# Kernel optimization log

Hardware: AMD Instinct MI355X
Metric: run time of the kernel (lower is better)

Reference implementation:

```python
import jax, jax.numpy as jnp
import numpy as np

D_MODEL = 1024
N_LAYERS = 4
EXPAND = 2
D_CONV = 4
D_STATE = 16
INTER = EXPAND * D_MODEL          # 2048
DT_RANK = (D_MODEL + 15) // 16    # 64, HF: math.ceil(d_model/16)
B_SZ = 4
SEQ = 1024
EPS = 1e-5


def setup_inputs() -> dict:
    key = jax.random.key(0)
    ks = jax.random.split(key, 8)
    nrm = lambda k, s: (0.02 * jax.random.normal(k, s)).astype(jnp.float32)
    return {
        "x": jax.random.normal(ks[0], (B_SZ, SEQ, D_MODEL), dtype=jnp.float32),
        "in_w": nrm(ks[1], (N_LAYERS, 2 * INTER, D_MODEL)),           # in_proj (no bias)
        "conv_w": nrm(ks[2], (N_LAYERS, INTER, D_CONV)),              # depthwise conv weight
        "conv_b": jnp.zeros((N_LAYERS, INTER), jnp.float32),           # conv bias
        "x_w": nrm(ks[3], (N_LAYERS, DT_RANK + 2 * D_STATE, INTER)),  # x_proj (no bias)
        "dt_w": nrm(ks[4], (N_LAYERS, INTER, DT_RANK)),               # dt_proj weight
        "dt_b": jax.random.uniform(ks[5], (N_LAYERS, INTER), minval=-4.0, maxval=-2.0).astype(jnp.float32),
        "A_log": jnp.tile(jnp.log(jnp.arange(1, D_STATE + 1, dtype=jnp.float32)), (N_LAYERS, INTER, 1)),
        "D": jnp.ones((N_LAYERS, INTER), jnp.float32),
        "out_w": nrm(ks[6], (N_LAYERS, D_MODEL, INTER)),              # out_proj (no bias)
        "norm_w": jnp.ones((N_LAYERS, D_MODEL), jnp.float32),          # per-block RMSNorm
        "norm_f_w": jnp.ones((D_MODEL,), jnp.float32),                 # final RMSNorm
    }


def _rmsnorm(x, w):
    return x * jax.lax.rsqrt(jnp.mean(x * x, axis=-1, keepdims=True) + EPS) * w


def _mixer(x, in_w, conv_w, conv_b, x_w, dt_w, dt_b, A_log, Dp, out_w):
    # x: [B, L, d_model]
    Bb = x.shape[0]
    proj = x @ in_w.T                              # [B, L, 2I]
    hs, gate = jnp.split(proj, 2, axis=-1)          # each [B, L, I]
    # causal depthwise conv over time
    hc = hs.transpose(0, 2, 1)                      # [B, I, L]
    hc = jnp.pad(hc, ((0, 0), (0, 0), (D_CONV - 1, 0)))
    hc = jax.lax.conv_general_dilated(
        hc, conv_w[:, None, :], (1,), 'VALID',
        dimension_numbers=('NCH', 'OIH', 'NCH'), feature_group_count=INTER)
    hc = hc + conv_b[None, :, None]
    u = jax.nn.silu(hc).transpose(0, 2, 1)          # [B, L, I]
    ssm = u @ x_w.T                                 # [B, L, dt_rank + 2N]
    dt, Bm, Cm = jnp.split(ssm, [DT_RANK, DT_RANK + D_STATE], axis=-1)
    dt = jax.nn.softplus(dt @ dt_w.T + dt_b)        # [B, L, I]
    A = -jnp.exp(A_log)                             # [I, N]

    def step(state, xs):
        dt_t, B_t, C_t, u_t = xs                    # [B,I], [B,N], [B,N], [B,I]
        dA = jnp.exp(dt_t[:, :, None] * A[None])    # [B, I, N]
        state = dA * state + (dt_t * u_t)[:, :, None] * B_t[:, None, :]
        y = jnp.einsum('bin,bn->bi', state, C_t)
        return state, y

    init = jnp.zeros((Bb, INTER, D_STATE), x.dtype)
    xs = (dt.transpose(1, 0, 2), Bm.transpose(1, 0, 2),
          Cm.transpose(1, 0, 2), u.transpose(1, 0, 2))
    _, ys = jax.lax.scan(step, init, xs)            # ys: [L, B, I]
    y = ys.transpose(1, 0, 2) + u * Dp              # skip term D * u
    y = y * jax.nn.silu(gate)
    return y @ out_w.T                              # [B, L, d_model]


def reference(x, in_w, conv_w, conv_b, x_w, dt_w, dt_b, A_log, D, out_w, norm_w, norm_f_w):
    h = x
    for l in range(N_LAYERS):
        h = h + _mixer(_rmsnorm(h, norm_w[l]), in_w[l], conv_w[l], conv_b[l],
                       x_w[l], dt_w[l], dt_b[l], A_log[l], D[l], out_w[l])
    return _rmsnorm(h, norm_f_w)
```

## Files before the change

### kernel.cpp

```cpp
#include <hip/hip_runtime.h>
#include <hip/hip_bf16.h>
#include <math.h>

#define D_MODEL 1024
#define N_LAYERS 4
#define INTER 2048
#define D_CONV 4
#define D_STATE 16
#define DT_RANK 64
#define B_SZ 4
#define SEQ 1024
#define TOK (B_SZ*SEQ)
#define XROWS 128
#define EPSV 1e-5f
#define GCH 64
#define TC (SEQ/GCH)
#define KSPL 4
#define OSPL 2

typedef unsigned short u16;
typedef unsigned int u32;
typedef __attribute__((ext_vector_type(8))) short bf16x8;
typedef __attribute__((ext_vector_type(4))) short s16x4;
typedef __attribute__((ext_vector_type(4))) float f32x4;

__device__ __forceinline__ u16 f2b(float f) {
    union { float f; unsigned u; } v; v.f = f;
    unsigned r = v.u + 0x7fffu + ((v.u >> 16) & 1u);
    return (u16)(r >> 16);
}
__device__ __forceinline__ float b2f(u16 h) {
    union { unsigned u; float f; } v; v.u = ((unsigned)h) << 16;
    return v.f;
}
__device__ __forceinline__ float silu(float x) {
    return x / (1.f + __expf(-x));
}
__device__ __forceinline__ void gload16(const void* g, void* l) {
    __builtin_amdgcn_global_load_lds(
        (const __attribute__((address_space(1))) void*)g,
        (__attribute__((address_space(3))) void*)l, 16, 0, 0);
}

__global__ __launch_bounds__(512, 2)
void gemm256_k(const u16* __restrict__ A, const u16* __restrict__ B,
               u16* __restrict__ C, int K, int ldc)
{
    __shared__ u16 lds[2][2][256 * 64];
    const int tid  = threadIdx.x;
    const int lane = tid & 63;
    const int wid  = tid >> 6;
    const int wr   = wid >> 2;
    const int wc   = wid & 3;
    const int row0 = blockIdx.y * 256;
    const int col0 = blockIdx.x * 256;
    const int r16   = lane & 15;
    const int khalf = lane >> 4;

    auto stage = [&](int buf, int k0) {
#pragma unroll
        for (int l = 0; l < 8; ++l) {
            int op = l >> 2;
            int c  = tid + (l & 3) * 512;
            int r  = c >> 3;
            int ds = c & 7;
            int sc = (ds ^ (r & 7)) * 8;
            const u16* src = op ? &B[(size_t)(col0 + r) * K + k0 + sc]
                                : &A[(size_t)(row0 + r) * K + k0 + sc];
            gload16(src, &lds[buf][op][c * 8]);
        }
    };
    auto rdA = [&](int buf, int mrow, int ks) -> bf16x8 {
        int row  = wr * 128 + mrow + r16;
        int phys = ((ks << 2) | khalf) ^ (row & 7);
        return *(const bf16x8*)&lds[buf][0][row * 64 + phys * 8];
    };
    auto rdB = [&](int buf, int nrow, int ks) -> bf16x8 {
        int row  = wc * 64 + nrow + r16;
        int phys = ((ks << 2) | khalf) ^ (row & 7);
        return *(const bf16x8*)&lds[buf][1][row * 64 + phys * 8];
    };

    f32x4 acc[8][4];
#pragma unroll
    for (int m = 0; m < 8; ++m)
#pragma unroll
        for (int n = 0; n < 4; ++n)
            acc[m][n] = (f32x4)0.f;

    bf16x8 af[4][2], bf2[2][2];

#define PHASE_MFMA(MH, NH, VMDRAIN) do {                                      \
    asm volatile("s_waitcnt lgkmcnt(0)" ::: "memory");                        \
    __builtin_amdgcn_sched_barrier(0);                                        \
    __builtin_amdgcn_s_setprio(1);                                            \
    _Pragma("unroll")                                                         \
    for (int ks = 0; ks < 2; ++ks)                                            \
        _Pragma("unroll")                                                     \
        for (int m = 0; m < 4; ++m)                                           \
            _Pragma("unroll")                                                 \
            for (int n = 0; n < 2; ++n)                                       \
                acc[(MH)*4+m][(NH)*2+n] =                                     \
                    __builtin_amdgcn_mfma_f32_16x16x32_bf16(                  \
                        af[m][ks], bf2[n][ks], acc[(MH)*4+m][(NH)*2+n],0,0,0);\
    __builtin_amdgcn_s_setprio(0);                                            \
    if (VMDRAIN) { asm volatile("s_waitcnt vmcnt(0)" ::: "memory"); }         \
    __builtin_amdgcn_s_barrier();                                             \
} while (0)

    const int nt = K >> 6;
    stage(0, 0);
    asm volatile("s_waitcnt vmcnt(0)" ::: "memory");
    __builtin_amdgcn_s_barrier();

    for (int j = 0; j < nt; ++j) {
        const int buf = j & 1;
        if (j + 1 < nt) stage(buf ^ 1, (j + 1) << 6);
#pragma unroll
        for (int m = 0; m < 4; ++m) {
            af[m][0] = rdA(buf, m * 16, 0); af[m][1] = rdA(buf, m * 16, 1);
        }
#pragma unroll
        for (int n = 0; n < 2; ++n) {
            bf2[n][0] = rdB(buf, n * 16, 0); bf2[n][1] = rdB(buf, n * 16, 1);
        }
        __builtin_amdgcn_s_barrier();
        PHASE_MFMA(0, 0, 0);
#pragma unroll
        for (int n = 0; n < 2; ++n) {
            bf2[n][0] = rdB(buf, 32 + n * 16, 0); bf2[n][1] = rdB(buf, 32 + n * 16, 1);
        }
        __builtin_amdgcn_s_barrier();
        PHASE_MFMA(0, 1, 0);
#pragma unroll
        for (int m = 0; m < 4; ++m) {
            af[m][0] = rdA(buf, 64 + m * 16, 0); af[m][1] = rdA(buf, 64 + m * 16, 1);
        }
        __builtin_amdgcn_s_barrier();
        PHASE_MFMA(1, 1, 0);
#pragma unroll
        for (int n = 0; n < 2; ++n) {
            bf2[n][0] = rdB(buf, n * 16, 0); bf2[n][1] = rdB(buf, n * 16, 1);
        }
        __builtin_amdgcn_s_barrier();
        PHASE_MFMA(1, 0, 1);
    }
#undef PHASE_MFMA

    const int orow = row0 + wr * 128;
    const int ocol = col0 + wc * 64;
#pragma unroll
    for (int am = 0; am < 8; ++am)
#pragma unroll
        for (int an = 0; an < 4; ++an)
#pragma unroll
            for (int r = 0; r < 4; ++r) {
                int rr = orow + am * 16 + khalf * 4 + r;
                int cc = ocol + an * 16 + r16;
                C[(size_t)rr * ldc + cc] = f2b(acc[am][an][r]);
            }
}

template<int EPI, int NPX = 1>
__global__ __launch_bounds__(256)
void gemm_bt(const u16* __restrict__ A, const u16* __restrict__ B,
             void* __restrict__ C, const float* __restrict__ aux,
             int K, int lda, int ldc, size_t pstride)
{
    __shared__ u16 As[3][128 * 32];
    __shared__ u16 Bs[3][128 * 32];
    const int tid  = threadIdx.x;
    const int lane = tid & 63;
    const int w    = tid >> 6;
    const int wr   = w >> 1, wc = w & 1;
    const int row0 = blockIdx.y * 128;
    int col0 = blockIdx.x * 128;
    if (EPI == 4) {
        int part = blockIdx.x / NPX;
        col0 = (blockIdx.x % NPX) * 128;
        A += (size_t)part * K;
        B += (size_t)part * K;
        C = (void*)((float*)C + (size_t)part * pstride);
    }
    const int r16   = lane & 15;
    const int khalf = lane >> 4;
    const int kslot = khalf ^ ((r16 >> 1) & 3);

    auto stage = [&](int buf, int k0) {
#pragma unroll
        for (int c = 0; c < 2; ++c) {
            int chunk = tid + c * 256;
            int r  = chunk >> 2;
            int j  = chunk & 3;
            int k8 = (j ^ ((r >> 1) & 3)) * 8;
            gload16(&A[(size_t)(row0 + r) * lda + k0 + k8], &As[buf][chunk * 8]);
            gload16(&B[(size_t)(col0 + r) * lda + k0 + k8], &Bs[buf][chunk * 8]);
        }
    };

    f32x4 acc[4][4];
#pragma unroll
    for (int m = 0; m < 4; ++m)
#pragma unroll
        for (int n = 0; n < 4; ++n)
            acc[m][n] = (f32x4)0.f;

    const int nt = K >> 5;
    stage(0, 0);
    if (nt > 1) stage(1, 32);

    int cur = 0, sb = 2;
    for (int t = 0; t < nt; ++t) {
        if (t + 2 < nt) {
            stage(sb, (t + 2) << 5);
            asm volatile("s_waitcnt vmcnt(8)" ::: "memory");
        } else if (t + 1 < nt) {
            asm volatile("s_waitcnt vmcnt(4)" ::: "memory");
        } else {
            asm volatile("s_waitcnt vmcnt(0)" ::: "memory");
        }
        __builtin_amdgcn_s_barrier();

        bf16x8 af[4], bfr[4];
#pragma unroll
        for (int m = 0; m < 4; ++m)
            af[m]  = *(const bf16x8*)&As[cur][(wr * 64 + m * 16 + r16) * 32 + kslot * 8];
#pragma unroll
        for (int n = 0; n < 4; ++n)
            bfr[n] = *(const bf16x8*)&Bs[cur][(wc * 64 + n * 16 + r16) * 32 + kslot * 8];
#pragma unroll
        for (int m = 0; m < 4; ++m)
#pragma unroll
            for (int n = 0; n < 4; ++n)
                acc[m][n] = __builtin_amdgcn_mfma_f32_16x16x32_bf16(
                    af[m], bfr[n], acc[m][n], 0, 0, 0);

        __builtin_amdgcn_sched_barrier(0);
        asm volatile("s_waitcnt lgkmcnt(0)" ::: "memory");
        __builtin_amdgcn_s_barrier();
        cur = (cur == 2) ? 0 : cur + 1;
        sb  = (sb  == 2) ? 0 : sb  + 1;
    }

    const int orow = row0 + wr * 64;
    const int ocol = col0 + wc * 64;
#pragma unroll
    for (int m = 0; m < 4; ++m)
#pragma unroll
        for (int n = 0; n < 4; ++n) {
#pragma unroll
            for (int r = 0; r < 4; ++r) {
                int rr = orow + m * 16 + khalf * 4 + r;
                int cc = ocol + n * 16 + r16;
                float v = acc[m][n][r];
                size_t o = (size_t)rr * ldc + cc;
                if (EPI == 0 || EPI == 4) {
                    ((float*)C)[o] = v;
                } else if (EPI == 2) {
                    float x = v + aux[cc];
                    float sp = (x > 20.f) ? x : log1pf(__expf(x));
                    ((u16*)C)[o] = f2b(sp);
                }
            }
        }
}

__global__ __launch_bounds__(256)
void xred_k(const float* __restrict__ part, float* __restrict__ ssm,
            u16* __restrict__ dtr)
{
    int idx = blockIdx.x * 256 + threadIdx.x;
    int row = idx >> 5;
    int col = (idx & 31) * 4;
    size_t o = (size_t)row * XROWS + col;
    const size_t stride = (size_t)TOK * XROWS;
    f32x4 v = *(const f32x4*)&part[o];
#pragma unroll
    for (int p = 1; p < KSPL; ++p)
        v += *(const f32x4*)&part[o + p * stride];
    *(f32x4*)&ssm[o] = v;
    if (col < DT_RANK) {
        s16x4 d;
#pragma unroll
        for (int j = 0; j < 4; ++j) d[j] = (short)f2b(v[j]);
        *(s16x4*)&dtr[(size_t)row * DT_RANK + col] = d;
    }
}

template<int OUTBF>
__global__ __launch_bounds__(256)
void rmsnorm_k(const float* __restrict__ in, const float* __restrict__ w,
               void* __restrict__ out)
{
    __shared__ float red[4];
    const int row = blockIdx.x;
    const int tid = threadIdx.x;
    const float* r = in + (size_t)row * D_MODEL;
    f32x4 v = *(const f32x4*)&r[tid * 4];
    float ss = v[0]*v[0] + v[1]*v[1] + v[2]*v[2] + v[3]*v[3];
#pragma unroll
    for (int m = 32; m >= 1; m >>= 1) ss += __shfl_xor(ss, m, 64);
    if ((tid & 63) == 0) red[tid >> 6] = ss;
    __syncthreads();
    if (tid == 0) {
        float s = red[0] + red[1] + red[2] + red[3];
        red[0] = rsqrtf(s / (float)D_MODEL + EPSV);
    }
    __syncthreads();
    float sc = red[0];
    if (OUTBF) {
        u16* o = (u16*)out + (size_t)row * D_MODEL + tid * 4;
#pragma unroll
        for (int j = 0; j < 4; ++j) o[j] = f2b(v[j] * sc * w[tid * 4 + j]);
    } else {
        float* o = (float*)out + (size_t)row * D_MODEL + tid * 4;
#pragma unroll
        for (int j = 0; j < 4; ++j) o[j] = v[j] * sc * w[tid * 4 + j];
    }
}

template<int OUTBF, int WRITEH>
__global__ __launch_bounds__(256)
void rmsnorm_res_k(const float* __restrict__ hin, const float* __restrict__ p,
                   const float* __restrict__ w, float* __restrict__ hout,
                   void* __restrict__ out)
{
    __shared__ float red[4];
    const int row = blockIdx.x;
    const int tid = threadIdx.x;
    const size_t o4 = (size_t)row * D_MODEL + tid * 4;
    f32x4 v  = *(const f32x4*)&hin[o4];
    f32x4 p0 = *(const f32x4*)&p[o4];
    f32x4 p1 = *(const f32x4*)&p[(size_t)TOK * D_MODEL + o4];
    v += p0 + p1;
    if (WRITEH) *(f32x4*)&hout[o4] = v;
    float ss = v[0]*v[0] + v[1]*v[1] + v[2]*v[2] + v[3]*v[3];
#pragma unroll
    for (int m = 32; m >= 1; m >>= 1) ss += __shfl_xor(ss, m, 64);
    if ((tid & 63) == 0) red[tid >> 6] = ss;
    __syncthreads();
    if (tid == 0) {
        float s = red[0] + red[1] + red[2] + red[3];
        red[0] = rsqrtf(s / (float)D_MODEL + EPSV);
    }
    __syncthreads();
    float sc = red[0];
    if (OUTBF) {
        u16* o = (u16*)out + o4;
#pragma unroll
        for (int j = 0; j < 4; ++j) o[j] = f2b(v[j] * sc * w[tid * 4 + j]);
    } else {
        float* o = (float*)out + o4;
#pragma unroll
        for (int j = 0; j < 4; ++j) o[j] = v[j] * sc * w[tid * 4 + j];
    }
}

__global__ __launch_bounds__(256)
void conv_silu_k(const u16* __restrict__ projbf, const float* __restrict__ w,
                 const float* __restrict__ bias, u16* __restrict__ ubf)
{
    const int row = blockIdx.x;
    const int t   = row & (SEQ - 1);
    const int i0  = threadIdx.x * 8;
    float acc[8];
    {
        f32x4 b0 = *(const f32x4*)&bias[i0];
        f32x4 b1 = *(const f32x4*)&bias[i0 + 4];
#pragma unroll
        for (int j = 0; j < 4; ++j) { acc[j] = b0[j]; acc[j + 4] = b1[j]; }
    }
    f32x4 wv[8];
#pragma unroll
    for (int j = 0; j < 8; ++j)
        wv[j] = *(const f32x4*)&w[(i0 + j) * 4];
#pragma unroll
    for (int k = 0; k < 4; ++k) {
        int tt = t - 3 + k;
        if (tt >= 0) {
            bf16x8 hv = *(const bf16x8*)&projbf[(size_t)(row - 3 + k) * 4096 + i0];
#pragma unroll
            for (int j = 0; j < 8; ++j)
                acc[j] += b2f((u16)hv[j]) * wv[j][k];
        }
    }
    bf16x8 o;
#pragma unroll
    for (int j = 0; j < 8; ++j)
        o[j] = (short)f2b(silu(acc[j]));
    *(bf16x8*)&ubf[(size_t)row * INTER + i0] = o;
}

__global__ __launch_bounds__(256)
void achk_k(const float* __restrict__ Alog, int* __restrict__ flags)
{
    int idx = blockIdx.x * 256 + threadIdx.x;
    if (idx >= N_LAYERS * INTER * D_STATE) return;
    int l = idx / (INTER * D_STATE);
    int n = idx & (D_STATE - 1);
    float ref = logf((float)(n + 1));
    if (fabsf(Alog[idx] - ref) > 1e-4f) atomicAnd(&flags[l], 0);
}

#define POWCH(W, p) \
    float p##2=(W)*(W), p##3=p##2*(W), p##4=p##2*p##2, p##5=p##4*(W),        \
          p##6=p##4*p##2, p##7=p##4*p##3, p##8=p##4*p##4, p##9=p##8*(W),     \
          p##10=p##8*p##2, p##11=p##8*p##3, p##12=p##8*p##4, p##13=p##8*p##5,\
          p##14=p##8*p##6, p##15=p##8*p##7, p##16=p##8*p##8;

#define SUPD(S, B, du, w1) \
    S[0]=w1*S[0]+du*B[0][0];   S[1]=w1##2*S[1]+du*B[0][1];                   \
    S[2]=w1##3*S[2]+du*B[0][2];  S[3]=w1##4*S[3]+du*B[0][3];                 \
    S[4]=w1##5*S[4]+du*B[1][0];  S[5]=w1##6*S[5]+du*B[1][1];                 \
    S[6]=w1##7*S[6]+du*B[1][2];  S[7]=w1##8*S[7]+du*B[1][3];                 \
    S[8]=w1##9*S[8]+du*B[2][0];  S[9]=w1##10*S[9]+du*B[2][1];                \
    S[10]=w1##11*S[10]+du*B[2][2]; S[11]=w1##12*S[11]+du*B[2][3];            \
    S[12]=w1##13*S[12]+du*B[3][0]; S[13]=w1##14*S[13]+du*B[3][1];            \
    S[14]=w1##15*S[14]+du*B[3][2]; S[15]=w1##16*S[15]+du*B[3][3];

#define YDOT(S, Cv) \
    (S[0]*Cv[0][0]+S[1]*Cv[0][1]+S[2]*Cv[0][2]+S[3]*Cv[0][3]                 \
    +S[4]*Cv[1][0]+S[5]*Cv[1][1]+S[6]*Cv[1][2]+S[7]*Cv[1][3]                 \
    +S[8]*Cv[2][0]+S[9]*Cv[2][1]+S[10]*Cv[2][2]+S[11]*Cv[2][3]               \
    +S[12]*Cv[3][0]+S[13]*Cv[3][1]+S[14]*Cv[3][2]+S[15]*Cv[3][3])

__global__ __launch_bounds__(256)
void scan1_k(const u16* __restrict__ dtbf, const u16* __restrict__ ubf,
             const float* __restrict__ ssm, const float* __restrict__ Alog,
             const int* __restrict__ flag,
             float* __restrict__ cst, float* __restrict__ dts)
{
    __shared__ float Bsh[TC][D_STATE];
    const int tid = threadIdx.x;
    const int i2  = blockIdx.x * 256 + tid;
    const int c0  = i2 * 2;
    const int g   = blockIdx.y;
    const int b   = blockIdx.z;
    const int t0  = g * TC;
    {
        int t = tid >> 4, n = tid & 15;
        Bsh[t][n] = ssm[(size_t)(b * SEQ + t0 + t) * XROWS + DT_RANK + n];
    }
    __syncthreads();

    float s0[D_STATE], s1[D_STATE];
#pragma unroll
    for (int n = 0; n < D_STATE; ++n) { s0[n] = 0.f; s1[n] = 0.f; }
    float ds0 = 0.f, ds1 = 0.f;

    const u32* dtp = (const u32*)dtbf + ((size_t)(b * SEQ + t0) * INTER >> 1) + i2;
    const u32* up  = (const u32*)ubf  + ((size_t)(b * SEQ + t0) * INTER >> 1) + i2;

    if (flag[0]) {
#pragma unroll
        for (int t = 0; t < TC; ++t) {
            u32 dp = dtp[(size_t)t * (INTER / 2)];
            u32 uq = up[(size_t)t * (INTER / 2)];
            float dta = b2f((u16)dp), dtb = b2f((u16)(dp >> 16));
            float ua  = b2f((u16)uq), ub  = b2f((u16)(uq >> 16));
            float dua = dta * ua, dub = dtb * ub;
            ds0 += dta; ds1 += dtb;
            float wa = __expf(-dta), wb = __expf(-dtb);
            POWCH(wa, wa) POWCH(wb, wb)
            const float (*Bv)[D_STATE] = nullptr; (void)Bv;
            f32x4 Bq[4];
#pragma unroll
            for (int q = 0; q < 4; ++q) Bq[q] = *(const f32x4*)&Bsh[t][q * 4];
            SUPD(s0, Bq, dua, wa)
            SUPD(s1, Bq, dub, wb)
        }
    } else {
        float a0[D_STATE], a1[D_STATE];
#pragma unroll
        for (int n = 0; n < D_STATE; ++n) {
            a0[n] = -__expf(Alog[(size_t)c0 * D_STATE + n]);
            a1[n] = -__expf(Alog[(size_t)(c0 + 1) * D_STATE + n]);
        }
        for (int t = 0; t < TC; ++t) {
            u32 dp = dtp[(size_t)t * (INTER / 2)];
            u32 uq = up[(size_t)t * (INTER / 2)];
            float dta = b2f((u16)dp), dtb = b2f((u16)(dp >> 16));
            float ua  = b2f((u16)uq), ub  = b2f((u16)(uq >> 16));
            float dua = dta * ua, dub = dtb * ub;
            ds0 += dta; ds1 += dtb;
#pragma unroll
            for (int n = 0; n < D_STATE; ++n) {
                float Bn = Bsh[t][n];
                s0[n] = __expf(dta * a0[n]) * s0[n] + dua * Bn;
                s1[n] = __expf(dtb * a1[n]) * s1[n] + dub * Bn;
            }
        }
    }
    size_t o = ((size_t)(b * GCH + g) * INTER + c0) * D_STATE;
#pragma unroll
    for (int n = 0; n < D_STATE; n += 4) {
        f32x4 v0 = { s0[n], s0[n+1], s0[n+2], s0[n+3] };
        f32x4 v1 = { s1[n], s1[n+1], s1[n+2], s1[n+3] };
        *(f32x4*)&cst[o + n] = v0;
        *(f32x4*)&cst[o + D_STATE + n] = v1;
    }
    size_t od = (size_t)(b * GCH + g) * INTER + c0;
    dts[od] = ds0; dts[od + 1] = ds1;
}

__global__ __launch_bounds__(256)
void scan2_k(float* __restrict__ cst, const float* __restrict__ dts,
             const float* __restrict__ Alog)
{
    int idx = blockIdx.x * 256 + threadIdx.x;
    int sub = idx & 3;
    int i   = (idx >> 2) & (INTER - 1);
    int b   = idx >> 13;
    int n0  = sub * 4;
    float a[4];
#pragma unroll
    for (int n = 0; n < 4; ++n)
        a[n] = -__expf(Alog[(size_t)i * D_STATE + n0 + n]);
    f32x4 s = (f32x4)0.f;
    for (int g = 0; g < GCH; ++g) {
        size_t o = ((size_t)(b * GCH + g) * INTER + i) * D_STATE + n0;
        f32x4 tmp = *(const f32x4*)&cst[o];
        *(f32x4*)&cst[o] = s;
        float d = dts[(size_t)(b * GCH + g) * INTER + i];
#pragma unroll
        for (int n = 0; n < 4; ++n)
            s[n] = __expf(a[n] * d) * s[n] + tmp[n];
    }
}

__global__ __launch_bounds__(256)
void scan3_k(const u16* __restrict__ dtbf, const u16* __restrict__ ubf,
             const float* __restrict__ ssm, const u16* __restrict__ projbf,
             const float* __restrict__ Alog, const float* __restrict__ Dp,
             const int* __restrict__ flag,
             const float* __restrict__ sst, u16* __restrict__ ybf)
{
    __shared__ float Bsh[TC][D_STATE];
    __shared__ float Csh[TC][D_STATE];
    const int tid = threadIdx.x;
    const int i2  = blockIdx.x * 256 + tid;
    const int c0  = i2 * 2;
    const int g   = blockIdx.y;
    const int b   = blockIdx.z;
    const int t0  = g * TC;
    {
        int t = tid >> 4, n = tid & 15;
        size_t row = (size_t)(b * SEQ + t0 + t) * XROWS;
        Bsh[t][n] = ssm[row + DT_RANK + n];
        Csh[t][n] = ssm[row + DT_RANK + D_STATE + n];
    }
    __syncthreads();

    const float Da = Dp[c0], Db = Dp[c0 + 1];
    float s0[D_STATE], s1[D_STATE];
    size_t so = ((size_t)(b * GCH + g) * INTER + c0) * D_STATE;
#pragma unroll
    for (int n = 0; n < D_STATE; n += 4) {
        f32x4 v0 = *(const f32x4*)&sst[so + n];
        f32x4 v1 = *(const f32x4*)&sst[so + D_STATE + n];
        s0[n] = v0[0]; s0[n+1] = v0[1]; s0[n+2] = v0[2]; s0[n+3] = v0[3];
        s1[n] = v1[0]; s1[n+1] = v1[1]; s1[n+2] = v1[2]; s1[n+3] = v1[3];
    }

    const u32* dtp = (const u32*)dtbf + ((size_t)(b * SEQ + t0) * INTER >> 1) + i2;
    const u32* up  = (const u32*)ubf  + ((size_t)(b * SEQ + t0) * INTER >> 1) + i2;
    const u32* gp  = (const u32*)projbf + (((size_t)(b * SEQ + t0) * 4096 + INTER) >> 1) + i2;
    u32*       yp  = (u32*)ybf + ((size_t)(b * SEQ + t0) * INTER >> 1) + i2;

    if (flag[0]) {
#pragma unroll
        for (int t = 0; t < TC; ++t) {
            u32 dp = dtp[(size_t)t * (INTER / 2)];
            u32 uq = up[(size_t)t * (INTER / 2)];
            u32 gq = gp[(size_t)t * (4096 / 2)];
            float dta = b2f((u16)dp), dtb = b2f((u16)(dp >> 16));
            float ua  = b2f((u16)uq), ub  = b2f((u16)(uq >> 16));
            float ga  = b2f((u16)gq), gb  = b2f((u16)(gq >> 16));
            float dua = dta * ua, dub = dtb * ub;
            float wa = __expf(-dta), wb = __expf(-dtb);
            POWCH(wa, wa) POWCH(wb, wb)
            f32x4 Bq[4], Cq[4];
#pragma unroll
            for (int q = 0; q < 4; ++q) {
                Bq[q] = *(const f32x4*)&Bsh[t][q * 4];
                Cq[q] = *(const f32x4*)&Csh[t][q * 4];
            }
            SUPD(s0, Bq, dua, wa)
            SUPD(s1, Bq, dub, wb)
            float y0 = YDOT(s0, Cq);
            float y1 = YDOT(s1, Cq);
            y0 = (y0 + Da * ua) * silu(ga);
            y1 = (y1 + Db * ub) * silu(gb);
            yp[(size_t)t * (INTER / 2)] = (u32)f2b(y0) | ((u32)f2b(y1) << 16);
        }
    } else {
        float a0[D_STATE], a1[D_STATE];
#pragma unroll
        for (int n = 0; n < D_STATE; ++n) {
            a0[n] = -__expf(Alog[(size_t)c0 * D_STATE + n]);
            a1[n] = -__expf(Alog[(size_t)(c0 + 1) * D_STATE + n]);
        }
        for (int t = 0; t < TC; ++t) {
            u32 dp = dtp[(size_t)t * (INTER / 2)];
            u32 uq = up[(size_t)t * (INTER / 2)];
            u32 gq = gp[(size_t)t * (4096 / 2)];
            float dta = b2f((u16)dp), dtb = b2f((u16)(dp >> 16));
            float ua  = b2f((u16)uq), ub  = b2f((u16)(uq >> 16));
            float ga  = b2f((u16)gq), gb  = b2f((u16)(gq >> 16));
            float dua = dta * ua, dub = dtb * ub;
            float y0 = 0.f, y1 = 0.f;
#pragma unroll
            for (int n = 0; n < D_STATE; ++n) {
                float Bn = Bsh[t][n], Cn = Csh[t][n];
                s0[n] = __expf(dta * a0[n]) * s0[n] + dua * Bn;
                s1[n] = __expf(dtb * a1[n]) * s1[n] + dub * Bn;
                y0 += s0[n] * Cn; y1 += s1[n] * Cn;
            }
            y0 = (y0 + Da * ua) * silu(ga);
            y1 = (y1 + Db * ub) * silu(gb);
            yp[(size_t)t * (INTER / 2)] = (u32)f2b(y0) | ((u32)f2b(y1) << 16);
        }
    }
}

__global__ __launch_bounds__(256)
void cvt_f2b_k(const float* __restrict__ in, u16* __restrict__ out, int n)
{
    int idx = blockIdx.x * 256 + threadIdx.x;
    if (idx < n) out[idx] = f2b(in[idx]);
}

__global__ __launch_bounds__(256)
void pad_xw_k(const float* __restrict__ xw, u16* __restrict__ out)
{
    int idx = blockIdx.x * 256 + threadIdx.x;
    if (idx >= N_LAYERS * XROWS * INTER) return;
    int l = idx / (XROWS * INTER);
    int r = (idx >> 11) & (XROWS - 1);
    int c = idx & (INTER - 1);
    out[idx] = (r < 96) ? f2b(xw[((size_t)l * 96 + r) * INTER + c]) : (u16)0;
}

extern "C" void kernel_launch(void* const* d_in, const int* in_sizes, int n_in,
                              void* d_out, int out_size, void* d_ws, size_t ws_size,
                              hipStream_t stream)
{
    const float* x      = (const float*)d_in[0];
    const float* in_w   = (const float*)d_in[1];
    const float* conv_w = (const float*)d_in[2];
    const float* conv_b = (const float*)d_in[3];
    const float* x_w    = (const float*)d_in[4];
    const float* dt_w   = (const float*)d_in[5];
    const float* dt_b   = (const float*)d_in[6];
    const float* A_log  = (const float*)d_in[7];
    const float* Dp     = (const float*)d_in[8];
    const float* out_w  = (const float*)d_in[9];
    const float* norm_w = (const float*)d_in[10];
    const float* norm_f = (const float*)d_in[11];

    char* ws = (char*)d_ws;
    size_t off = 0;
    auto alloc = [&](size_t bytes) { char* p = ws + off; off += (bytes + 255) & ~(size_t)255; return p; };

    u16*   inw_bf  = (u16*)  alloc((size_t)N_LAYERS * 4096 * 1024 * 2);
    u16*   xw_bf   = (u16*)  alloc((size_t)N_LAYERS * XROWS * INTER * 2);
    u16*   dtw_bf  = (u16*)  alloc((size_t)N_LAYERS * INTER * DT_RANK * 2);
    u16*   outw_bf = (u16*)  alloc((size_t)N_LAYERS * D_MODEL * INTER * 2);
    float* h       = (float*)alloc((size_t)TOK * D_MODEL * 4);
    u16*   xn_bf   = (u16*)  alloc((size_t)TOK * D_MODEL * 2);
    u16*   proj_bf = (u16*)  alloc((size_t)TOK * 4096 * 2);
    u16*   u_bf    = (u16*)  alloc((size_t)TOK * INTER * 2);
    float* ssm     = (float*)alloc((size_t)TOK * XROWS * 4);
    float* parts   = (float*)alloc((size_t)OSPL * TOK * D_MODEL * 4);
    u16*   dtr_bf  = (u16*)  alloc((size_t)TOK * DT_RANK * 2);
    u16*   dt_bf   = (u16*)  alloc((size_t)TOK * INTER * 2);
    u16*   y_bf    = (u16*)  alloc((size_t)TOK * INTER * 2);
    float* cst     = (float*)alloc((size_t)B_SZ * GCH * INTER * D_STATE * 4);
    float* dts     = (float*)alloc((size_t)B_SZ * GCH * INTER * 4);
    int*   aflags  = (int*)  alloc(N_LAYERS * sizeof(int));
    (void)ws_size; (void)n_in; (void)in_sizes; (void)out_size;

    {
        int n = N_LAYERS * 4096 * 1024;
        cvt_f2b_k<<<n / 256, 256, 0, stream>>>(in_w, inw_bf, n);
        int np = N_LAYERS * XROWS * INTER;
        pad_xw_k<<<np / 256, 256, 0, stream>>>(x_w, xw_bf);
        int nd = N_LAYERS * INTER * DT_RANK;
        cvt_f2b_k<<<nd / 256, 256, 0, stream>>>(dt_w, dtw_bf, nd);
        int no = N_LAYERS * D_MODEL * INTER;
        cvt_f2b_k<<<no / 256, 256, 0, stream>>>(out_w, outw_bf, no);
        hipMemsetAsync(aflags, 0xFF, N_LAYERS * sizeof(int), stream);
        int na = N_LAYERS * INTER * D_STATE;
        achk_k<<<(na + 255) / 256, 256, 0, stream>>>(A_log, aflags);
    }

    for (int l = 0; l < N_LAYERS; ++l) {
        if (l == 0)
            rmsnorm_k<1><<<TOK, 256, 0, stream>>>(x, norm_w, xn_bf);
        else
            rmsnorm_res_k<1, 1><<<TOK, 256, 0, stream>>>(
                (l == 1) ? x : h, parts, norm_w + (size_t)l * D_MODEL, h, xn_bf);
        gemm256_k<<<dim3(16, 16), 512, 0, stream>>>(
            xn_bf, inw_bf + (size_t)l * 4096 * 1024, proj_bf, 1024, 4096);
        conv_silu_k<<<TOK, 256, 0, stream>>>(
            proj_bf, conv_w + (size_t)l * INTER * D_CONV, conv_b + (size_t)l * INTER, u_bf);
        gemm_bt<4, 1><<<dim3(KSPL, 32), 256, 0, stream>>>(
            u_bf, xw_bf + (size_t)l * XROWS * INTER, parts, nullptr,
            INTER / KSPL, INTER, XROWS, (size_t)TOK * XROWS);
        xred_k<<<(TOK * 32) / 256, 256, 0, stream>>>(parts, ssm, dtr_bf);
        gemm_bt<2><<<dim3(16, 32), 256, 0, stream>>>(
            dtr_bf, dtw_bf + (size_t)l * INTER * DT_RANK, dt_bf,
            dt_b + (size_t)l * INTER, DT_RANK, DT_RANK, INTER, 0);
        scan1_k<<<dim3(INTER / 512, GCH, B_SZ), 256, 0, stream>>>(
            dt_bf, u_bf, ssm, A_log + (size_t)l * INTER * D_STATE, aflags + l, cst, dts);
        scan2_k<<<(B_SZ * INTER * 4) / 256, 256, 0, stream>>>(
            cst, dts, A_log + (size_t)l * INTER * D_STATE);
        scan3_k<<<dim3(INTER / 512, GCH, B_SZ), 256, 0, stream>>>(
            dt_bf, u_bf, ssm, proj_bf, A_log + (size_t)l * INTER * D_STATE,
            Dp + (size_t)l * INTER, aflags + l, cst, y_bf);
        gemm_bt<4, 8><<<dim3(OSPL * 8, 32), 256, 0, stream>>>(
            y_bf, outw_bf + (size_t)l * D_MODEL * INTER, parts, nullptr,
            INTER / OSPL, INTER, D_MODEL, (size_t)TOK * D_MODEL);
    }
    rmsnorm_res_k<0, 0><<<TOK, 256, 0, stream>>>(
        h, parts, norm_f, nullptr, d_out);
}
```

Before: 940.1 us.

## Shrink in_proj GEMM tile to 256x128 with K=32 stages and raise occupancy

Reworks the in_proj GEMM from a 256x256 tile with K=64 per stage to a 256x128 tile with K=32 per stage. Each of the 8 waves now computes 64x64 outputs instead of 128x64, and the launch bound asks for 4 blocks per CU. The grid doubles to 512 blocks, so more of the MI355X's CUs get work and LDS per block drops to make room for the extra blocks. The x_proj split-K factor also goes from 4 to 8, which gives that GEMM more parallelism at the cost of more partial sums for the reduction kernel to add up. The tradeoff is less data reuse per tile and more barriers for each unit of K.

```diff
diff --git a/kernel.cpp b/kernel.cpp
--- a/kernel.cpp
+++ b/kernel.cpp
@@ -15,7 +15,7 @@
 #define EPSV 1e-5f
 #define GCH 64
 #define TC (SEQ/GCH)
-#define KSPL 4
+#define KSPL 8
 #define OSPL 2
 
 typedef unsigned short u16;
@@ -42,122 +42,107 @@
         (__attribute__((address_space(3))) void*)l, 16, 0, 0);
 }
 
-__global__ __launch_bounds__(512, 2)
+__global__ __launch_bounds__(512, 4)
 void gemm256_k(const u16* __restrict__ A, const u16* __restrict__ B,
                u16* __restrict__ C, int K, int ldc)
 {
-    __shared__ u16 lds[2][2][256 * 64];
+    __shared__ u16 ldsA[2][256 * 32];
+    __shared__ u16 ldsB[2][128 * 32];
     const int tid  = threadIdx.x;
     const int lane = tid & 63;
     const int wid  = tid >> 6;
-    const int wr   = wid >> 2;
-    const int wc   = wid & 3;
+    const int wrM  = wid >> 1;
+    const int wcN  = wid & 1;
     const int row0 = blockIdx.y * 256;
-    const int col0 = blockIdx.x * 256;
+    const int col0 = blockIdx.x * 128;
     const int r16   = lane & 15;
     const int khalf = lane >> 4;
 
     auto stage = [&](int buf, int k0) {
 #pragma unroll
-        for (int l = 0; l < 8; ++l) {
-            int op = l >> 2;
-            int c  = tid + (l & 3) * 512;
-            int r  = c >> 3;
-            int ds = c & 7;
-            int sc = (ds ^ (r & 7)) * 8;
-            const u16* src = op ? &B[(size_t)(col0 + r) * K + k0 + sc]
-                                : &A[(size_t)(row0 + r) * K + k0 + sc];
-            gload16(src, &lds[buf][op][c * 8]);
+        for (int l = 0; l < 3; ++l) {
+            int c = tid + l * 512;
+            if (c < 1024) {
+                int r  = c >> 2;
+                int ds = c & 3;
+                int sc = (ds ^ (r & 3)) * 8;
+                gload16(&A[(size_t)(row0 + r) * K + k0 + sc], &ldsA[buf][c * 8]);
+            } else {
+                int cb = c - 1024;
+                int r  = cb >> 2;
+                int ds = cb & 3;
+                int sc = (ds ^ (r & 3)) * 8;
+                gload16(&B[(size_t)(col0 + r) * K + k0 + sc], &ldsB[buf][cb * 8]);
+            }
         }
     };
-    auto rdA = [&](int buf, int mrow, int ks) -> bf16x8 {
-        int row  = wr * 128 + mrow + r16;
-        int phys = ((ks << 2) | khalf) ^ (row & 7);
-        return *(const bf16x8*)&lds[buf][0][row * 64 + phys * 8];
+    auto rdA = [&](int buf, int m) -> bf16x8 {
+        int row  = wrM * 64 + m * 16 + r16;
+        int phys = khalf ^ (row & 3);
+        return *(const bf16x8*)&ldsA[buf][row * 32 + phys * 8];
     };
-    auto rdB = [&](int buf, int nrow, int ks) -> bf16x8 {
-        int row  = wc * 64 + nrow + r16;
-        int phys = ((ks << 2) | khalf) ^ (row & 7);
-        return *(const bf16x8*)&lds[buf][1][row * 64 + phys * 8];
+    auto rdB = [&](int buf, int n) -> bf16x8 {
+        int row  = wcN * 64 + n * 16 + r16;
+        int phys = khalf ^ (row & 3);
+        return *(const bf16x8*)&ldsB[buf][row * 32 + phys * 8];
     };
 
-    f32x4 acc[8][4];
-#pragma unroll
-    for (int m = 0; m < 8; ++m)
+    f32x4 acc[4][4];
+#pragma unroll
+    for (int m = 0; m < 4; ++m)
 #pragma unroll
         for (int n = 0; n < 4; ++n)
             acc[m][n] = (f32x4)0.f;
 
-    bf16x8 af[4][2], bf2[2][2];
-
-#define PHASE_MFMA(MH, NH, VMDRAIN) do {                                      \
+    bf16x8 af[4], bfr[2];
+
+#define PHASE_MFMA(NH, VMDRAIN) do {                                          \
     asm volatile("s_waitcnt lgkmcnt(0)" ::: "memory");                        \
     __builtin_amdgcn_sched_barrier(0);                                        \
     __builtin_amdgcn_s_setprio(1);                                            \
     _Pragma("unroll")                                                         \
-    for (int ks = 0; ks < 2; ++ks)                                            \
+    for (int m = 0; m < 4; ++m)                                               \
         _Pragma("unroll")                                                     \
-        for (int m = 0; m < 4; ++m)                                           \
-            _Pragma("unroll")                                                 \
-            for (int n = 0; n < 2; ++n)                                       \
-                acc[(MH)*4+m][(NH)*2+n] =                                     \
-                    __builtin_amdgcn_mfma_f32_16x16x32_bf16(                  \
-                        af[m][ks], bf2[n][ks], acc[(MH)*4+m][(NH)*2+n],0,0,0);\
+        for (int n = 0; n < 2; ++n)                                           \
+            acc[m][(NH)*2+n] = __builtin_amdgcn_mfma_f32_16x16x32_bf16(       \
+                af[m], bfr[n], acc[m][(NH)*2+n], 0, 0, 0);                    \
     __builtin_amdgcn_s_setprio(0);                                            \
     if (VMDRAIN) { asm volatile("s_waitcnt vmcnt(0)" ::: "memory"); }         \
     __builtin_amdgcn_s_barrier();                                             \
 } while (0)
 
-    const int nt = K >> 6;
+    const int nt = K >> 5;
     stage(0, 0);
     asm volatile("s_waitcnt vmcnt(0)" ::: "memory");
     __builtin_amdgcn_s_barrier();
 
     for (int j = 0; j < nt; ++j) {
         const int buf = j & 1;
-        if (j + 1 < nt) stage(buf ^ 1, (j + 1) << 6);
-#pragma unroll
-        for (int m = 0; m < 4; ++m) {
-            af[m][0] = rdA(buf, m * 16, 0); af[m][1] = rdA(buf, m * 16, 1);
-        }
-#pragma unroll
-        for (int n = 0; n < 2; ++n) {
-            bf2[n][0] = rdB(buf, n * 16, 0); bf2[n][1] = rdB(buf, n * 16, 1);
-        }
+        if (j + 1 < nt) stage(buf ^ 1, (j + 1) << 5);
+#pragma unroll
+        for (int m = 0; m < 4; ++m) af[m] = rdA(buf, m);
+#pragma unroll
+        for (int n = 0; n < 2; ++n) bfr[n] = rdB(buf, n);
         __builtin_amdgcn_s_barrier();
-        PHASE_MFMA(0, 0, 0);
-#pragma unroll
-        for (int n = 0; n < 2; ++n) {
-            bf2[n][0] = rdB(buf, 32 + n * 16, 0); bf2[n][1] = rdB(buf, 32 + n * 16, 1);
-        }
+        PHASE_MFMA(0, 0);
+#pragma unroll
+        for (int n = 0; n < 2; ++n) bfr[n] = rdB(buf, 2 + n);
         __builtin_amdgcn_s_barrier();
-        PHASE_MFMA(0, 1, 0);
-#pragma unroll
-        for (int m = 0; m < 4; ++m) {
-            af[m][0] = rdA(buf, 64 + m * 16, 0); af[m][1] = rdA(buf, 64 + m * 16, 1);
-        }
-        __builtin_amdgcn_s_barrier();
-        PHASE_MFMA(1, 1, 0);
-#pragma unroll
-        for (int n = 0; n < 2; ++n) {
-            bf2[n][0] = rdB(buf, n * 16, 0); bf2[n][1] = rdB(buf, n * 16, 1);
-        }
-        __builtin_amdgcn_s_barrier();
-        PHASE_MFMA(1, 0, 1);
+        PHASE_MFMA(1, 1);
     }
 #undef PHASE_MFMA
 
-    const int orow = row0 + wr * 128;
-    const int ocol = col0 + wc * 64;
-#pragma unroll
-    for (int am = 0; am < 8; ++am)
-#pragma unroll
-        for (int an = 0; an < 4; ++an)
+    const int orow = row0 + wrM * 64;
+    const int ocol = col0 + wcN * 64;
+#pragma unroll
+    for (int m = 0; m < 4; ++m)
+#pragma unroll
+        for (int n = 0; n < 4; ++n)
 #pragma unroll
             for (int r = 0; r < 4; ++r) {
-                int rr = orow + am * 16 + khalf * 4 + r;
-                int cc = ocol + an * 16 + r16;
-                C[(size_t)rr * ldc + cc] = f2b(acc[am][an][r]);
+                int rr = orow + m * 16 + khalf * 4 + r;
+                int cc = ocol + n * 16 + r16;
+                C[(size_t)rr * ldc + cc] = f2b(acc[m][n][r]);
             }
 }
 
@@ -462,7 +447,6 @@
             ds0 += dta; ds1 += dtb;
             float wa = __expf(-dta), wb = __expf(-dtb);
             POWCH(wa, wa) POWCH(wb, wb)
-            const float (*Bv)[D_STATE] = nullptr; (void)Bv;
             f32x4 Bq[4];
 #pragma unroll
             for (int q = 0; q < 4; ++q) Bq[q] = *(const f32x4*)&Bsh[t][q * 4];
@@ -700,7 +684,7 @@
         else
             rmsnorm_res_k<1, 1><<<TOK, 256, 0, stream>>>(
                 (l == 1) ? x : h, parts, norm_w + (size_t)l * D_MODEL, h, xn_bf);
-        gemm256_k<<<dim3(16, 16), 512, 0, stream>>>(
+        gemm256_k<<<dim3(32, 16), 512, 0, stream>>>(
             xn_bf, inw_bf + (size_t)l * 4096 * 1024, proj_bf, 1024, 4096);
         conv_silu_k<<<TOK, 256, 0, stream>>>(
             proj_bf, conv_w + (size_t)l * INTER * D_CONV, conv_b + (size_t)l * INTER, u_bf);
```

Result: no change. 951.5 us (+1.2%).
